# Kernel optimization log

Measured on AMD Instinct MI355X. Metric: run time of the kernel, lower is better.

Reference implementation:

```python
import jax, jax.numpy as jnp
import numpy as np
import math

NUM_HEADS = 16


def _alibi_slopes(n):
    # n is a power of 2 here (16)
    start = 2.0 ** (-2.0 ** (-(math.log2(n) - 3)))
    return jnp.asarray([start * (start ** i) for i in range(n)], dtype=jnp.float32)


def setup_inputs() -> dict:
    key = jax.random.key(0)
    ks = jax.random.split(key, 7)
    B, S, D = 2, 2048, 1024
    s = 0.02
    return {
        "query": jax.random.normal(ks[0], (B, S, D), jnp.float32),
        "key": jax.random.normal(ks[1], (B, S, D), jnp.float32),
        "value": jax.random.normal(ks[2], (B, S, D), jnp.float32),
        "Wq": jax.random.normal(ks[3], (D, D), jnp.float32) * s,
        "Wk": jax.random.normal(ks[4], (D, D), jnp.float32) * s,
        "Wv": jax.random.normal(ks[5], (D, D), jnp.float32) * s,
        "Wo": jax.random.normal(ks[6], (D, D), jnp.float32) * s,
    }


def reference(query, key, value, Wq, Wk, Wv, Wo):
    B, S, D = query.shape
    H = NUM_HEADS
    hd = D // H
    scale = math.sqrt(hd)

    # projections (bias-free linears), split into heads: [B, S, H, hd]
    Q = (query @ Wq).reshape(B, S, H, hd)
    K = (key @ Wk).reshape(B, -1, H, hd)
    V = (value @ Wv).reshape(B, -1, H, hd)

    # attention scores [B, H, S, S]
    scores = jnp.einsum("bqhd,bkhd->bhqk", Q, K) / scale

    # ALiBi bias: -slope_h * |i - j|, broadcast over batch
    pos = jnp.arange(S, dtype=jnp.float32)
    rel = jnp.abs(pos[None, :] - pos[:, None])  # [S, S]
    slopes = _alibi_slopes(H)
    scores = scores - slopes[None, :, None, None] * rel[None, None, :, :]

    attn = jax.nn.softmax(scores, axis=-1)
    out = jnp.einsum("bhqk,bkhd->bqhd", attn, V).reshape(B, S, D)
    return out @ Wo
```

## Files before the change

kernel.cpp:

```cpp
#include <hip/hip_runtime.h>
#include <cstdint>
#include <cstddef>


typedef unsigned short u16;
typedef __attribute__((ext_vector_type(8))) _Float16 half8;
typedef __attribute__((ext_vector_type(8))) unsigned short u16x8;
typedef __attribute__((ext_vector_type(4))) float f32x4;

#define DEVI static __device__ __forceinline__
#define MFMA16(a, b, c) __builtin_amdgcn_mfma_f32_16x16x32_f16(a, b, c, 0, 0, 0)

DEVI u16 f2h_bits(float f) {
  _Float16 h = (_Float16)f;
  union { _Float16 h; u16 u; } v; v.h = h;
  return v.u;
}

DEVI void gl_lds16(const u16* g, u16* l) {
  __builtin_amdgcn_global_load_lds(
      (const __attribute__((address_space(1))) void*)g,
      (__attribute__((address_space(3))) void*)l, 16, 0, 0);
}

__global__ __launch_bounds__(256) void cast3_h(const float* __restrict__ in0,
                                               const float* __restrict__ in1,
                                               const float* __restrict__ in2,
                                               u16* __restrict__ o0,
                                               u16* __restrict__ o1,
                                               u16* __restrict__ o2, int n) {
  const float* in = blockIdx.z == 0 ? in0 : (blockIdx.z == 1 ? in1 : in2);
  u16* out = blockIdx.z == 0 ? o0 : (blockIdx.z == 1 ? o1 : o2);
  int i = (blockIdx.x * 256 + threadIdx.x) * 4;
  if (i + 3 < n) {
    const float4 v = *(const float4*)(in + i);
    ushort4 o;
    o.x = f2h_bits(v.x); o.y = f2h_bits(v.y); o.z = f2h_bits(v.z); o.w = f2h_bits(v.w);
    *(ushort4*)(out + i) = o;
  }
}

__global__ __launch_bounds__(256) void transpose4_h(
    const float* __restrict__ W0, const float* __restrict__ W1,
    const float* __restrict__ W2, const float* __restrict__ W3,
    u16* __restrict__ T0, u16* __restrict__ T1, u16* __restrict__ T2,
    u16* __restrict__ T3) {
  const float* W = blockIdx.z == 0 ? W0 : (blockIdx.z == 1 ? W1 : (blockIdx.z == 2 ? W2 : W3));
  u16* Wt = blockIdx.z == 0 ? T0 : (blockIdx.z == 1 ? T1 : (blockIdx.z == 2 ? T2 : T3));
  __shared__ float tile[32][33];
  const int bx = blockIdx.x * 32;
  const int by = blockIdx.y * 32;
  const int x = threadIdx.x & 31;
  const int y0 = threadIdx.x >> 5;
#pragma unroll
  for (int i = y0; i < 32; i += 8)
    tile[i][x] = W[(size_t)(by + i) * 1024 + bx + x];
  __syncthreads();
#pragma unroll
  for (int i = y0; i < 32; i += 8)
    Wt[(size_t)(bx + i) * 1024 + by + x] = f2h_bits(tile[x][i]);
}

__global__ __launch_bounds__(256) void vtrans(const u16* __restrict__ Vp,
                                              u16* __restrict__ Vt) {
  __shared__ u16 tile[64][72];
  const int t = threadIdx.x;
  const int s0 = blockIdx.x * 64;
  const int bh = blockIdx.y;
  const int b = bh >> 4, h = bh & 15;
#pragma unroll
  for (int it = 0; it < 2; ++it) {
    const int ci = it * 256 + t;
    const int srow = ci >> 3, cc = (ci & 7) << 3;
    const u16x8 v = *(const u16x8*)(Vp + (size_t)(b * 2048 + s0 + srow) * 1024 + h * 64 + cc);
    *(u16x8*)(&tile[srow][cc]) = v;
  }
  __syncthreads();
#pragma unroll
  for (int it = 0; it < 2; ++it) {
    const int ci = it * 256 + t;
    const int drow = ci >> 3, cc = (ci & 7) << 3;
    u16x8 o;
#pragma unroll
    for (int j = 0; j < 8; ++j) o[j] = tile[cc + j][drow];
    *(u16x8*)(Vt + ((size_t)bh * 64 + drow) * 2048 + s0 + cc) = o;
  }
}

DEVI void gemm_body(const u16* __restrict__ A, const u16* __restrict__ Bt,
                    void* __restrict__ Cout, int mode, int kLo, int kHi,
                    u16* As, u16* Bs) {
  constexpr int K = 1024, N = 1024;
  const int t = threadIdx.x;
  const int lane = t & 63;
  const int quad = lane >> 4;
  const int l16 = lane & 15;
  const int wid = t >> 6;
  const int mBase = blockIdx.y * 128;
  const int nBase = blockIdx.x * 128;
  const int wM = (wid >> 1) * 64;
  const int wN = (wid & 1) * 64;
  const int cswz = l16 & 7;

  f32x4 acc[4][4];
#pragma unroll
  for (int i = 0; i < 4; ++i)
#pragma unroll
    for (int j = 0; j < 4; ++j) acc[i][j] = (f32x4){0.f, 0.f, 0.f, 0.f};

  for (int kt = kLo; kt < kHi; ++kt) {
    const int kB = kt * 64;
    __syncthreads();
#pragma unroll
    for (int i = 0; i < 4; ++i) {
      const int ci = i * 256 + t;
      const int row = ci >> 3;
      const int col = (((ci & 7) ^ (row & 7)) << 3);
      gl_lds16(A + (size_t)(mBase + row) * K + kB + col, As + ci * 8);
      gl_lds16(Bt + (size_t)(nBase + row) * K + kB + col, Bs + ci * 8);
    }
    __syncthreads();

#pragma unroll
    for (int kk = 0; kk < 2; ++kk) {
      const int ck = (((kk * 4 + quad) ^ cswz) << 3);
      half8 a[4], b[4];
#pragma unroll
      for (int mi = 0; mi < 4; ++mi)
        a[mi] = *(const half8*)(As + (wM + mi * 16 + l16) * 64 + ck);
#pragma unroll
      for (int ni = 0; ni < 4; ++ni)
        b[ni] = *(const half8*)(Bs + (wN + ni * 16 + l16) * 64 + ck);
#pragma unroll
      for (int mi = 0; mi < 4; ++mi)
#pragma unroll
        for (int ni = 0; ni < 4; ++ni)
          acc[mi][ni] = MFMA16(a[mi], b[ni], acc[mi][ni]);
    }
  }

#pragma unroll
  for (int mi = 0; mi < 4; ++mi) {
#pragma unroll
    for (int ni = 0; ni < 4; ++ni) {
#pragma unroll
      for (int r = 0; r < 4; ++r) {
        const int m = mBase + wM + mi * 16 + quad * 4 + r;
        const int n = nBase + wN + ni * 16 + l16;
        const float v = acc[mi][ni][r];
        if (mode == 0) {
          ((float*)Cout)[(size_t)m * N + n] = v;
        } else if (mode == 1) {
          ((u16*)Cout)[(size_t)m * N + n] = f2h_bits(v);
        } else {
          atomicAdd((float*)Cout + (size_t)m * N + n, v);
        }
      }
    }
  }
}

__global__ __launch_bounds__(256) void proj_qkv(
    const u16* __restrict__ qb, const u16* __restrict__ kb, const u16* __restrict__ vb,
    const u16* __restrict__ Wqt, const u16* __restrict__ Wkt, const u16* __restrict__ Wvt,
    u16* __restrict__ Qp, u16* __restrict__ Kp, u16* __restrict__ Vp) {
  __shared__ u16 As[128 * 64];
  __shared__ u16 Bs[128 * 64];
  const int z = blockIdx.z;
  const u16* A = z == 0 ? qb : (z == 1 ? kb : vb);
  const u16* Bt = z == 0 ? Wqt : (z == 1 ? Wkt : Wvt);
  void* C = z == 0 ? (void*)Qp : (z == 1 ? (void*)Kp : (void*)Vp);
  gemm_body(A, Bt, C, 1, 0, 16, As, Bs);
}

__global__ __launch_bounds__(256) void gemm_out(const u16* __restrict__ Ao,
                                                const u16* __restrict__ Wot,
                                                float* __restrict__ out) {
  __shared__ u16 As[128 * 64];
  __shared__ u16 Bs[128 * 64];
  const int z = blockIdx.z;
  gemm_body(Ao, Wot, out, 3, z * 8, z * 8 + 8, As, Bs);
}

__global__ __launch_bounds__(128, 2) void flash_alibi(
    const u16* __restrict__ Qg, const u16* __restrict__ Kg,
    const u16* __restrict__ Vtg, u16* __restrict__ Og) {
  constexpr int S = 2048, Dm = 1024, HD = 64;
  __shared__ u16 Qs[64 * 64];
  __shared__ u16 Ks[2][64 * 64];
  __shared__ u16 Vs[2][64 * 64];
  __shared__ u16 Ps[64 * 64];
  const int t = threadIdx.x, lane = t & 63, wid = t >> 6;
  const int quad = lane >> 4, l16 = lane & 15;
  const int idx = blockIdx.x;
  const int h = 15 - (idx >> 6);
  const int qt = (idx >> 1) & 31;
  const int b = idx & 1;
  const int qBase = qt * 64;
  const size_t qRow0 = (size_t)b * S + qBase;
  const float sl2 = __builtin_amdgcn_exp2f(-0.5f * (float)(h + 1)) * 1.44269504f;
  const float sc2 = 0.125f * 1.44269504f;
  const int Di = (int)(22.0f / sl2);
  const int ktLo = max(0, (qBase - Di) >> 6);
  const int ktHi = min(31, (qBase + 63 + Di) >> 6);
  const int cswz = ((l16 & 7) << 3);
  const u16* Kgb = Kg + (size_t)b * S * Dm + h * HD;
  const u16* Vgb = Vtg + (size_t)(b * 16 + h) * HD * S;

#pragma unroll
  for (int i = 0; i < 4; ++i) {
    const int ci = i * 128 + t;
    const int row = ci >> 3, col = (((ci & 7) ^ (row & 7)) << 3);
    gl_lds16(Qg + (qRow0 + row) * Dm + h * HD + col, Qs + ci * 8);
  }
#pragma unroll
  for (int i = 0; i < 4; ++i) {
    const int ci = i * 128 + t;
    const int row = ci >> 3, col = (((ci & 7) ^ (row & 7)) << 3);
    gl_lds16(Kgb + (size_t)(ktLo * 64 + row) * Dm + col, Ks[0] + ci * 8);
    gl_lds16(Vgb + (size_t)row * S + ktLo * 64 + col, Vs[0] + ci * 8);
  }

  float bi[2][4];
#pragma unroll
  for (int m = 0; m < 2; ++m)
#pragma unroll
    for (int r = 0; r < 4; ++r)
      bi[m][r] = sl2 * (float)(qBase + wid * 32 + m * 16 + quad * 4 + r);

  f32x4 acc_o[2][4];
#pragma unroll
  for (int m = 0; m < 2; ++m)
#pragma unroll
    for (int nd = 0; nd < 4; ++nd) acc_o[m][nd] = (f32x4){0.f, 0.f, 0.f, 0.f};
  float lrow[2][4] = {{0.f, 0.f, 0.f, 0.f}, {0.f, 0.f, 0.f, 0.f}};

  const int pRowBase = wid * 32;
  int cur = 0;

  for (int kt = ktLo; kt <= ktHi; ++kt, cur ^= 1) {
    __asm__ volatile("s_waitcnt vmcnt(0) lgkmcnt(0)\n\ts_barrier" ::: "memory");

    if (kt < ktHi) {
      const int kB2 = (kt + 1) * 64;
      u16* Kd = Ks[cur ^ 1];
      u16* Vd = Vs[cur ^ 1];
#pragma unroll
      for (int i = 0; i < 4; ++i) {
        const int ci = i * 128 + t;
        const int row = ci >> 3, col = (((ci & 7) ^ (row & 7)) << 3);
        gl_lds16(Kgb + (size_t)(kB2 + row) * Dm + col, Kd + ci * 8);
        gl_lds16(Vgb + (size_t)row * S + kB2 + col, Vd + ci * 8);
      }
    }

    const int kB = kt * 64;
    f32x4 s[2][4];
#pragma unroll
    for (int m = 0; m < 2; ++m)
#pragma unroll
      for (int ni = 0; ni < 4; ++ni) s[m][ni] = (f32x4){0.f, 0.f, 0.f, 0.f};
#pragma unroll
    for (int ks = 0; ks < 2; ++ks) {
      const int ck = ((ks * 4 + quad) << 3) ^ cswz;
      const half8 a0 = *(const half8*)(Qs + (wid * 32 + l16) * HD + ck);
      const half8 a1 = *(const half8*)(Qs + (wid * 32 + 16 + l16) * HD + ck);
#pragma unroll
      for (int ni = 0; ni < 4; ++ni) {
        const half8 bk = *(const half8*)(Ks[cur] + (ni * 16 + l16) * HD + ck);
        s[0][ni] = MFMA16(a0, bk, s[0][ni]);
        s[1][ni] = MFMA16(a1, bk, s[1][ni]);
      }
    }

    float bj[4];
#pragma unroll
    for (int ni = 0; ni < 4; ++ni) bj[ni] = sl2 * (float)(kB + ni * 16 + l16);
#pragma unroll
    for (int m = 0; m < 2; ++m) {
#pragma unroll
      for (int r = 0; r < 4; ++r) {
        float rs = 0.f;
        const int prow = (pRowBase + m * 16 + quad * 4 + r) * 64;
#pragma unroll
        for (int ni = 0; ni < 4; ++ni) {
          const float d = fabsf(bi[m][r] - bj[ni]);
          const float p = __builtin_amdgcn_exp2f(s[m][ni][r] * sc2 - d);
          rs += p;
          Ps[prow + ((ni * 16 + l16) ^ (quad << 4))] = f2h_bits(p);
        }
        lrow[m][r] += rs;
      }
    }
    __asm__ volatile("s_waitcnt lgkmcnt(0)" ::: "memory");

#pragma unroll
    for (int ks = 0; ks < 2; ++ks) {
      const int pk = (ks * 32 + quad * 8) ^ ((l16 & 12) << 2);
      const int ck = ((ks * 4 + quad) << 3) ^ cswz;
      const half8 aP0 = *(const half8*)(Ps + (pRowBase + l16) * 64 + pk);
      const half8 aP1 = *(const half8*)(Ps + (pRowBase + 16 + l16) * 64 + pk);
#pragma unroll
      for (int nd = 0; nd < 4; ++nd) {
        const half8 bv = *(const half8*)(Vs[cur] + (nd * 16 + l16) * HD + ck);
        acc_o[0][nd] = MFMA16(aP0, bv, acc_o[0][nd]);
        acc_o[1][nd] = MFMA16(aP1, bv, acc_o[1][nd]);
      }
    }
  }

#pragma unroll
  for (int m = 0; m < 2; ++m) {
#pragma unroll
    for (int r = 0; r < 4; ++r) {
      float l = lrow[m][r];
      l += __shfl_xor(l, 1);
      l += __shfl_xor(l, 2);
      l += __shfl_xor(l, 4);
      l += __shfl_xor(l, 8);
      const float inv = 1.f / l;
      const int rloc = wid * 32 + m * 16 + quad * 4 + r;
#pragma unroll
      for (int nd = 0; nd < 4; ++nd)
        Og[(qRow0 + rloc) * Dm + h * HD + nd * 16 + l16] = f2h_bits(acc_o[m][nd][r] * inv);
    }
  }
}

extern "C" void kernel_launch(void* const* d_in, const int* in_sizes, int n_in,
                              void* d_out, int out_size, void* d_ws, size_t ws_size,
                              hipStream_t stream) {
  const float* q  = (const float*)d_in[0];
  const float* k  = (const float*)d_in[1];
  const float* v  = (const float*)d_in[2];
  const float* Wq = (const float*)d_in[3];
  const float* Wk = (const float*)d_in[4];
  const float* Wv = (const float*)d_in[5];
  const float* Wo = (const float*)d_in[6];
  char* ws = (char*)d_ws;
  const size_t MB = 1ull << 20;
  u16* qb  = (u16*)(ws + 0 * MB);
  u16* kb  = (u16*)(ws + 8 * MB);
  u16* vb  = (u16*)(ws + 16 * MB);
  u16* Wqt = (u16*)(ws + 24 * MB);
  u16* Wkt = (u16*)(ws + 26 * MB);
  u16* Wvt = (u16*)(ws + 28 * MB);
  u16* Wot = (u16*)(ws + 30 * MB);
  u16* Qp  = (u16*)(ws + 32 * MB);
  u16* Kp  = (u16*)(ws + 40 * MB);
  u16* Vp  = (u16*)(ws + 48 * MB);
  u16* Ao  = (u16*)(ws + 56 * MB);
  u16* Vt  = vb;

  const int n = 2 * 2048 * 1024;
  hipMemsetAsync(d_out, 0, (size_t)out_size * 4, stream);
  cast3_h<<<dim3(n / 1024, 1, 3), 256, 0, stream>>>(q, k, v, qb, kb, vb, n);
  transpose4_h<<<dim3(32, 32, 4), 256, 0, stream>>>(Wq, Wk, Wv, Wo, Wqt, Wkt, Wvt, Wot);
  proj_qkv<<<dim3(8, 32, 3), 256, 0, stream>>>(qb, kb, vb, Wqt, Wkt, Wvt, Qp, Kp, Vp);
  vtrans<<<dim3(32, 32), 256, 0, stream>>>(Vp, Vt);
  flash_alibi<<<1024, 128, 0, stream>>>(Qp, Kp, Vt, Ao);
  gemm_out<<<dim3(8, 32, 2), 256, 0, stream>>>(Ao, Wot, (float*)d_out);
}
```

Measured before the change: 262.0 us.

## Split long-window ALiBi heads across KV segments and merge partials; replace atomics

```diff
diff --git a/kernel.cpp b/kernel.cpp
--- a/kernel.cpp
+++ b/kernel.cpp
@@ -150,10 +150,8 @@
         const float v = acc[mi][ni][r];
         if (mode == 0) {
           ((float*)Cout)[(size_t)m * N + n] = v;
-        } else if (mode == 1) {
+        } else {
           ((u16*)Cout)[(size_t)m * N + n] = f2h_bits(v);
-        } else {
-          atomicAdd((float*)Cout + (size_t)m * N + n, v);
         }
       }
     }
@@ -175,16 +173,30 @@
 
 __global__ __launch_bounds__(256) void gemm_out(const u16* __restrict__ Ao,
                                                 const u16* __restrict__ Wot,
-                                                float* __restrict__ out) {
+                                                float* __restrict__ p0,
+                                                float* __restrict__ p1) {
   __shared__ u16 As[128 * 64];
   __shared__ u16 Bs[128 * 64];
   const int z = blockIdx.z;
-  gemm_body(Ao, Wot, out, 3, z * 8, z * 8 + 8, As, Bs);
+  gemm_body(Ao, Wot, z ? (void*)p1 : (void*)p0, 0, z * 8, z * 8 + 8, As, Bs);
+}
+
+__global__ __launch_bounds__(256) void add2(const float* __restrict__ a,
+                                            const float* __restrict__ b,
+                                            float* __restrict__ o, int n) {
+  int i = (blockIdx.x * 256 + threadIdx.x) * 4;
+  if (i + 3 < n) {
+    float4 x = *(const float4*)(a + i);
+    const float4 y = *(const float4*)(b + i);
+    x.x += y.x; x.y += y.y; x.z += y.z; x.w += y.w;
+    *(float4*)(o + i) = x;
+  }
 }
 
 __global__ __launch_bounds__(128, 2) void flash_alibi(
     const u16* __restrict__ Qg, const u16* __restrict__ Kg,
-    const u16* __restrict__ Vtg, u16* __restrict__ Og) {
+    const u16* __restrict__ Vtg, u16* __restrict__ Opart,
+    float* __restrict__ lpart) {
   constexpr int S = 2048, Dm = 1024, HD = 64;
   __shared__ u16 Qs[64 * 64];
   __shared__ u16 Ks[2][64 * 64];
@@ -193,9 +205,18 @@
   const int t = threadIdx.x, lane = t & 63, wid = t >> 6;
   const int quad = lane >> 4, l16 = lane & 15;
   const int idx = blockIdx.x;
-  const int h = 15 - (idx >> 6);
-  const int qt = (idx >> 1) & 31;
-  const int b = idx & 1;
+  const int s = 29 - (idx >> 6);
+  const int bq = idx & 63;
+  const int b = bq >> 5, qt = bq & 31;
+  int h, seg, nseg;
+  if      (s >= 26) { h = 15; seg = s - 26; nseg = 4; }
+  else if (s >= 22) { h = 14; seg = s - 22; nseg = 4; }
+  else if (s >= 18) { h = 13; seg = s - 18; nseg = 4; }
+  else if (s >= 15) { h = 12; seg = s - 15; nseg = 3; }
+  else if (s >= 13) { h = 11; seg = s - 13; nseg = 2; }
+  else if (s >= 11) { h = 10; seg = s - 11; nseg = 2; }
+  else if (s >= 9)  { h = 9;  seg = s - 9;  nseg = 2; }
+  else              { h = s;  seg = 0;      nseg = 1; }
   const int qBase = qt * 64;
   const size_t qRow0 = (size_t)b * S + qBase;
   const float sl2 = __builtin_amdgcn_exp2f(-0.5f * (float)(h + 1)) * 1.44269504f;
@@ -203,6 +224,10 @@
   const int Di = (int)(22.0f / sl2);
   const int ktLo = max(0, (qBase - Di) >> 6);
   const int ktHi = min(31, (qBase + 63 + Di) >> 6);
+  const int W = ktHi - ktLo + 1;
+  const int myLo = ktLo + (W * seg) / nseg;
+  const int myHi = ktLo + (W * (seg + 1)) / nseg - 1;
+  const size_t slotG = (size_t)bq * 30 + s;
   const int cswz = ((l16 & 7) << 3);
   const u16* Kgb = Kg + (size_t)b * S * Dm + h * HD;
   const u16* Vgb = Vtg + (size_t)(b * 16 + h) * HD * S;
@@ -213,12 +238,14 @@
     const int row = ci >> 3, col = (((ci & 7) ^ (row & 7)) << 3);
     gl_lds16(Qg + (qRow0 + row) * Dm + h * HD + col, Qs + ci * 8);
   }
-#pragma unroll
-  for (int i = 0; i < 4; ++i) {
-    const int ci = i * 128 + t;
-    const int row = ci >> 3, col = (((ci & 7) ^ (row & 7)) << 3);
-    gl_lds16(Kgb + (size_t)(ktLo * 64 + row) * Dm + col, Ks[0] + ci * 8);
-    gl_lds16(Vgb + (size_t)row * S + ktLo * 64 + col, Vs[0] + ci * 8);
+  if (myLo <= myHi) {
+#pragma unroll
+    for (int i = 0; i < 4; ++i) {
+      const int ci = i * 128 + t;
+      const int row = ci >> 3, col = (((ci & 7) ^ (row & 7)) << 3);
+      gl_lds16(Kgb + (size_t)(myLo * 64 + row) * Dm + col, Ks[0] + ci * 8);
+      gl_lds16(Vgb + (size_t)row * S + myLo * 64 + col, Vs[0] + ci * 8);
+    }
   }
 
   float bi[2][4];
@@ -238,10 +265,10 @@
   const int pRowBase = wid * 32;
   int cur = 0;
 
-  for (int kt = ktLo; kt <= ktHi; ++kt, cur ^= 1) {
+  for (int kt = myLo; kt <= myHi; ++kt, cur ^= 1) {
     __asm__ volatile("s_waitcnt vmcnt(0) lgkmcnt(0)\n\ts_barrier" ::: "memory");
 
-    if (kt < ktHi) {
+    if (kt < myHi) {
       const int kB2 = (kt + 1) * 64;
       u16* Kd = Ks[cur ^ 1];
       u16* Vd = Vs[cur ^ 1];
@@ -255,11 +282,11 @@
     }
 
     const int kB = kt * 64;
-    f32x4 s[2][4];
+    f32x4 sc[2][4];
 #pragma unroll
     for (int m = 0; m < 2; ++m)
 #pragma unroll
-      for (int ni = 0; ni < 4; ++ni) s[m][ni] = (f32x4){0.f, 0.f, 0.f, 0.f};
+      for (int ni = 0; ni < 4; ++ni) sc[m][ni] = (f32x4){0.f, 0.f, 0.f, 0.f};
 #pragma unroll
     for (int ks = 0; ks < 2; ++ks) {
       const int ck = ((ks * 4 + quad) << 3) ^ cswz;
@@ -268,8 +295,8 @@
 #pragma unroll
       for (int ni = 0; ni < 4; ++ni) {
         const half8 bk = *(const half8*)(Ks[cur] + (ni * 16 + l16) * HD + ck);
-        s[0][ni] = MFMA16(a0, bk, s[0][ni]);
-        s[1][ni] = MFMA16(a1, bk, s[1][ni]);
+        sc[0][ni] = MFMA16(a0, bk, sc[0][ni]);
+        sc[1][ni] = MFMA16(a1, bk, sc[1][ni]);
       }
     }
 
@@ -285,7 +312,7 @@
 #pragma unroll
         for (int ni = 0; ni < 4; ++ni) {
           const float d = fabsf(bi[m][r] - bj[ni]);
-          const float p = __builtin_amdgcn_exp2f(s[m][ni][r] * sc2 - d);
+          const float p = __builtin_amdgcn_exp2f(sc[m][ni][r] * sc2 - d);
           rs += p;
           Ps[prow + ((ni * 16 + l16) ^ (quad << 4))] = f2h_bits(p);
         }
@@ -318,13 +345,58 @@
       l += __shfl_xor(l, 2);
       l += __shfl_xor(l, 4);
       l += __shfl_xor(l, 8);
-      const float inv = 1.f / l;
       const int rloc = wid * 32 + m * 16 + quad * 4 + r;
+      if (l16 == 0) lpart[slotG * 64 + rloc] = l;
 #pragma unroll
       for (int nd = 0; nd < 4; ++nd)
-        Og[(qRow0 + rloc) * Dm + h * HD + nd * 16 + l16] = f2h_bits(acc_o[m][nd][r] * inv);
-    }
-  }
+        Opart[slotG * 4096 + rloc * 64 + nd * 16 + l16] = f2h_bits(acc_o[m][nd][r]);
+    }
+  }
+}
+
+__global__ __launch_bounds__(256) void flash_merge(
+    const u16* __restrict__ Opart, const float* __restrict__ lpart,
+    u16* __restrict__ Ao) {
+  const int idx = blockIdx.x;
+  const int h = idx & 15, bq = idx >> 4;
+  const int b = bq >> 5, qt = bq & 31;
+  int base, nseg;
+  if      (h == 15) { base = 26; nseg = 4; }
+  else if (h == 14) { base = 22; nseg = 4; }
+  else if (h == 13) { base = 18; nseg = 4; }
+  else if (h == 12) { base = 15; nseg = 3; }
+  else if (h == 11) { base = 13; nseg = 2; }
+  else if (h == 10) { base = 11; nseg = 2; }
+  else if (h == 9)  { base = 9;  nseg = 2; }
+  else              { base = h;  nseg = 1; }
+  const int t = threadIdx.x;
+  const int q = t >> 2, dB = (t & 3) * 16;
+  float acc[16];
+#pragma unroll
+  for (int j = 0; j < 16; ++j) acc[j] = 0.f;
+  float l = 0.f;
+  for (int sg = 0; sg < nseg; ++sg) {
+    const size_t slotG = (size_t)bq * 30 + base + sg;
+    l += lpart[slotG * 64 + q];
+    const u16* p = Opart + slotG * 4096 + q * 64 + dB;
+    const half8 v0 = *(const half8*)p;
+    const half8 v1 = *(const half8*)(p + 8);
+#pragma unroll
+    for (int j = 0; j < 8; ++j) {
+      acc[j] += (float)v0[j];
+      acc[8 + j] += (float)v1[j];
+    }
+  }
+  const float inv = 1.f / l;
+  u16x8 o0, o1;
+#pragma unroll
+  for (int j = 0; j < 8; ++j) {
+    o0[j] = f2h_bits(acc[j] * inv);
+    o1[j] = f2h_bits(acc[8 + j] * inv);
+  }
+  u16* dst = Ao + ((size_t)(b * 2048 + qt * 64 + q)) * 1024 + h * 64 + dB;
+  *(u16x8*)dst = o0;
+  *(u16x8*)(dst + 8) = o1;
 }
 
 extern "C" void kernel_launch(void* const* d_in, const int* in_sizes, int n_in,
@@ -351,13 +423,18 @@
   u16* Vp  = (u16*)(ws + 48 * MB);
   u16* Ao  = (u16*)(ws + 56 * MB);
   u16* Vt  = vb;
+  u16*   Opart = (u16*)(ws + 0 * MB);
+  float* lpart = (float*)(ws + 48 * MB);
+  float* p0 = (float*)(ws + 0 * MB);
+  float* p1 = (float*)(ws + 32 * MB);
 
   const int n = 2 * 2048 * 1024;
-  hipMemsetAsync(d_out, 0, (size_t)out_size * 4, stream);
   cast3_h<<<dim3(n / 1024, 1, 3), 256, 0, stream>>>(q, k, v, qb, kb, vb, n);
   transpose4_h<<<dim3(32, 32, 4), 256, 0, stream>>>(Wq, Wk, Wv, Wo, Wqt, Wkt, Wvt, Wot);
   proj_qkv<<<dim3(8, 32, 3), 256, 0, stream>>>(qb, kb, vb, Wqt, Wkt, Wvt, Qp, Kp, Vp);
   vtrans<<<dim3(32, 32), 256, 0, stream>>>(Vp, Vt);
-  flash_alibi<<<1024, 128, 0, stream>>>(Qp, Kp, Vt, Ao);
-  gemm_out<<<dim3(8, 32, 2), 256, 0, stream>>>(Ao, Wot, (float*)d_out);
-}
+  flash_alibi<<<1920, 128, 0, stream>>>(Qp, Kp, Vt, Opart, lpart);
+  flash_merge<<<1024, 256, 0, stream>>>(Opart, lpart, Ao);
+  gemm_out<<<dim3(8, 32, 2), 256, 0, stream>>>(Ao, Wot, p0, p1);
+  add2<<<4096, 256, 0, stream>>>(p0, p1, (float*)d_out, n);
+}
```

New measurement: 245.9 us. 1.07x faster.
